# Optimization experiments

Hardware: AMD Instinct MI355X
Metric: run time of the kernel (lower is better)

Reference implementation:

```python
import jax, jax.numpy as jnp
import numpy as np

B, D, NH, HD, L, P, FF = 2, 256, 8, 32, 4, 4, 1024
SPATIAL = np.array([[100, 100], [50, 50], [25, 25], [13, 13]], dtype=np.int64)
S_TOTAL = int(SPATIAL.prod(1).sum())  # 13294
EPS = 1e-5


def setup_inputs() -> dict:
    key = jax.random.key(0)
    ks = jax.random.split(key, 20)
    std = 0.02
    f32 = jnp.float32
    return {
        "query": jax.random.normal(ks[0], (B, S_TOTAL, D), f32),
        "query_pos": jax.random.normal(ks[1], (B, S_TOTAL, D), f32),
        "valid_ratios": jnp.ones((B, L, 2), f32),
        "spatial_shapes": SPATIAL,
        "level_start_index": np.concatenate([[0], SPATIAL.prod(1).cumsum()[:-1]]).astype(np.int64),
        "W_off": jax.random.normal(ks[2], (D, NH * L * P * 2), f32) * std,
        "b_off": jax.random.normal(ks[3], (NH * L * P * 2,), f32) * std,
        "W_attn": jax.random.normal(ks[4], (D, NH * L * P), f32) * std,
        "b_attn": jax.random.normal(ks[5], (NH * L * P,), f32) * std,
        "W_val": jax.random.normal(ks[6], (D, D), f32) * std,
        "b_val": jnp.zeros((D,), f32),
        "W_out": jax.random.normal(ks[7], (D, D), f32) * std,
        "b_out": jnp.zeros((D,), f32),
        "ln1_g": jnp.ones((D,), f32),
        "ln1_b": jnp.zeros((D,), f32),
        "W1": jax.random.normal(ks[8], (D, FF), f32) * std,
        "b1": jnp.zeros((FF,), f32),
        "W2": jax.random.normal(ks[9], (FF, D), f32) * std,
        "b2": jnp.zeros((D,), f32),
        "ln2_g": jnp.ones((D,), f32),
        "ln2_b": jnp.zeros((D,), f32),
    }


def _layer_norm(x, g, b):
    m = x.mean(-1, keepdims=True)
    v = ((x - m) ** 2).mean(-1, keepdims=True)
    return (x - m) * jax.lax.rsqrt(v + EPS) * g + b


def _bilinear_sample(v, loc, H, W):
    # v: [B, NH, H*W, HD]; loc: [B, NH, S, P, 2] normalized to [0,1]
    # Matches F.grid_sample(bilinear, padding_mode='zeros', align_corners=False)
    x = loc[..., 0] * W - 0.5
    y = loc[..., 1] * H - 0.5
    x0 = jnp.floor(x)
    y0 = jnp.floor(y)
    lx, ly = x - x0, y - y0
    x0i = x0.astype(jnp.int32)
    y0i = y0.astype(jnp.int32)
    x1i, y1i = x0i + 1, y0i + 1

    def corner(yi, xi, w):
        valid = (xi >= 0) & (xi < W) & (yi >= 0) & (yi < H)
        idx = jnp.clip(yi, 0, H - 1) * W + jnp.clip(xi, 0, W - 1)  # [B,NH,S,P]
        b_, h_, s_, p_ = idx.shape
        g = jnp.take_along_axis(v, idx.reshape(b_, h_, s_ * p_)[..., None], axis=2)
        g = g.reshape(b_, h_, s_, p_, -1)
        return g * (w * valid)[..., None]

    return (corner(y0i, x0i, (1 - lx) * (1 - ly)) + corner(y0i, x1i, lx * (1 - ly))
            + corner(y1i, x0i, (1 - lx) * ly) + corner(y1i, x1i, lx * ly))


def _forward(query, query_pos, valid_ratios, spatial_shapes,
             W_off, b_off, W_attn, b_attn, W_val, b_val, W_out, b_out,
             ln1_g, ln1_b, W1, b1, W2, b2, ln2_g, ln2_b):
    ss = np.asarray(spatial_shapes)
    Bq, S, _ = query.shape

    # ----- reference points (per-pixel centers, normalized by valid ratios) -----
    refs = []
    for lvl in range(ss.shape[0]):
        H, W = int(ss[lvl, 0]), int(ss[lvl, 1])
        ry, rx = jnp.meshgrid(jnp.linspace(0.5, H - 0.5, H), jnp.linspace(0.5, W - 0.5, W), indexing='ij')
        vy = valid_ratios[:, lvl, 1][:, None, None]
        vx = valid_ratios[:, lvl, 0][:, None, None]
        ry = ry[None] / (vy * H)
        rx = rx[None] / (vx * W)
        refs.append(jnp.stack((rx, ry), -1).reshape(Bq, H * W, 2))
    ref = jnp.concatenate(refs, 1)  # [B, S, 2] (identical across levels)

    # ----- multi-scale deformable attention -----
    q = query + query_pos
    v = (query @ W_val + b_val).reshape(Bq, S, NH, HD).transpose(0, 2, 1, 3)  # [B,NH,S,HD]
    off = (q @ W_off + b_off).reshape(Bq, S, NH, L, P, 2)
    aw = jax.nn.softmax((q @ W_attn + b_attn).reshape(Bq, S, NH, L * P), -1)
    aw = aw.reshape(Bq, S, NH, L, P)
    normalizer = jnp.asarray(ss[:, ::-1].copy(), jnp.float32)  # (W, H) per level
    loc = ref[:, :, None, None, None, :] + off / normalizer[None, None, None, :, None, :]  # [B,S,NH,L,P,2]

    starts = np.concatenate([[0], ss.prod(1).cumsum()[:-1]])
    out = jnp.zeros((Bq, NH, S, HD), query.dtype)
    for lvl in range(ss.shape[0]):
        H, W = int(ss[lvl, 0]), int(ss[lvl, 1])
        s0 = int(starts[lvl])
        v_l = v[:, :, s0:s0 + H * W]                       # [B,NH,HW,HD]
        loc_l = loc[:, :, :, lvl].transpose(0, 2, 1, 3, 4)  # [B,NH,S,P,2]
        samp = _bilinear_sample(v_l, loc_l, H, W)           # [B,NH,S,P,HD]
        w_l = aw[:, :, :, lvl].transpose(0, 2, 1, 3)        # [B,NH,S,P]
        out = out + (samp * w_l[..., None]).sum(3)
    attn_out = out.transpose(0, 2, 1, 3).reshape(Bq, S, D) @ W_out + b_out

    # ----- residual + LN + FFN + residual + LN -----
    x = _layer_norm(query + attn_out, ln1_g, ln1_b)
    f = jax.nn.relu(x @ W1 + b1) @ W2 + b2
    return _layer_norm(x + f, ln2_g, ln2_b)


def reference(query, query_pos, valid_ratios, spatial_shapes, level_start_index,
              W_off, b_off, W_attn, b_attn, W_val, b_val, W_out, b_out,
              ln1_g, ln1_b, W1, b1, W2, b2, ln2_g, ln2_b):
    return _forward(query, query_pos, valid_ratios, spatial_shapes,
                    W_off, b_off, W_attn, b_attn, W_val, b_val, W_out, b_out,
                    ln1_g, ln1_b, W1, b1, W2, b2, ln2_g, ln2_b)
```

## Files before the change

kernel.cpp:

```cpp
#include <hip/hip_runtime.h>
#include <math.h>

#define R_ROWS 26588
#define S_TOT  13294
#define NHEAD  8
#define NLVL   4
#define EPSF   1e-5f

typedef __attribute__((ext_vector_type(8))) short short8;
typedef __attribute__((ext_vector_type(4))) float f32x4;
typedef __attribute__((ext_vector_type(2))) float f32x2;
typedef unsigned short ushort_t;

__device__ __forceinline__ unsigned short f2bf(float f) {
    unsigned int u = __builtin_bit_cast(unsigned int, f);
    unsigned int r = (u + 0x7FFFu + ((u >> 16) & 1u)) >> 16;
    return (unsigned short)r;
}

__global__ __launch_bounds__(256) void transpose_all_kernel(
    const float* __restrict__ W_val, const float* __restrict__ W_off,
    const float* __restrict__ W_attn, const float* __restrict__ W_out,
    const float* __restrict__ W1, const float* __restrict__ W2,
    ushort_t* __restrict__ wt_val, ushort_t* __restrict__ wt_off,
    ushort_t* __restrict__ wt_attn, ushort_t* __restrict__ wt_out,
    ushort_t* __restrict__ wt_w1, ushort_t* __restrict__ wt_w2)
{
    int bid = blockIdx.x;
    const float* src; ushort_t* dst; int K, N, t;
    if (bid < 64)       { src = W_val;  dst = wt_val;  K = 256;  N = 256;  t = bid; }
    else if (bid < 128) { src = W_off;  dst = wt_off;  K = 256;  N = 256;  t = bid - 64; }
    else if (bid < 160) { src = W_attn; dst = wt_attn; K = 256;  N = 128;  t = bid - 128; }
    else if (bid < 224) { src = W_out;  dst = wt_out;  K = 256;  N = 256;  t = bid - 160; }
    else if (bid < 480) { src = W1;     dst = wt_w1;   K = 256;  N = 1024; t = bid - 224; }
    else                { src = W2;     dst = wt_w2;   K = 1024; N = 256;  t = bid - 480; }
    int nt = N / 32;
    int bn = (t % nt) * 32, bk = (t / nt) * 32;

    __shared__ ushort_t tt[32][33];
    int x = threadIdx.x & 31;
    int y = threadIdx.x >> 5;
#pragma unroll
    for (int i = 0; i < 4; ++i) {
        int k = y + i * 8;
        tt[x][k] = f2bf(src[(long)(bk + k) * N + bn + x]);
    }
    __syncthreads();
#pragma unroll
    for (int i = 0; i < 4; ++i) {
        int n = y + i * 8;
        dst[(long)(bn + n) * K + bk + x] = tt[n][x];
    }
}

__global__ __launch_bounds__(256) void addcvt_kernel(
    const float* __restrict__ q, const float* __restrict__ p,
    ushort_t* __restrict__ qry_bf, ushort_t* __restrict__ qsum_bf, int n4)
{
    int i = blockIdx.x * 256 + threadIdx.x;
    if (i >= n4) return;
    float4 a = ((const float4*)q)[i];
    float4 b = ((const float4*)p)[i];
    uint2 qa, qs;
    qa.x = (unsigned)f2bf(a.x) | ((unsigned)f2bf(a.y) << 16);
    qa.y = (unsigned)f2bf(a.z) | ((unsigned)f2bf(a.w) << 16);
    qs.x = (unsigned)f2bf(a.x + b.x) | ((unsigned)f2bf(a.y + b.y) << 16);
    qs.y = (unsigned)f2bf(a.z + b.z) | ((unsigned)f2bf(a.w + b.w) << 16);
    ((uint2*)qry_bf)[i] = qa;
    ((uint2*)qsum_bf)[i] = qs;
}

__device__ __forceinline__ void stage32_async(
    const ushort_t* __restrict__ src_row0, int ld, int k0,
    ushort_t* lds, int wave, int lane)
{
#pragma unroll
    for (int inst = 0; inst < 2; ++inst) {
        int base_row = wave * 32 + inst * 16;
        int r = base_row + (lane >> 2);
        int quadS = lane & 3;
        int quadG = quadS ^ ((r >> 1) & 3);
        const ushort_t* gp = src_row0 + (long)r * ld + k0 + quadG * 8;
        __builtin_amdgcn_global_load_lds(
            (const __attribute__((address_space(1))) unsigned int*)gp,
            (__attribute__((address_space(3))) unsigned int*)&lds[base_row * 32],
            16, 0, 0);
    }
}

__device__ __forceinline__ void gemm_body(
    ushort_t* As, ushort_t* Bs,
    const ushort_t* __restrict__ A, const ushort_t* __restrict__ Wt,
    const float* __restrict__ bias, void* __restrict__ Cv,
    int M, int N, int K, int bm, int bn, bool out_bf16, bool relu)
{
    const int tid  = threadIdx.x;
    const int wave = tid >> 6;
    const int lane = tid & 63;
    const int l15  = lane & 15;
    const int quad = lane >> 4;
    const int wm   = (wave >> 1) * 64;
    const int wn   = (wave & 1) * 64;

    const ushort_t* Arow = A + (long)bm * K;
    const ushort_t* Brow = Wt + (long)bn * K;

    f32x4 acc[4][4];
#pragma unroll
    for (int i = 0; i < 4; ++i)
#pragma unroll
        for (int j = 0; j < 4; ++j) acc[i][j] = (f32x4)0.0f;

    int aoff[4], boff[4];
#pragma unroll
    for (int mi = 0; mi < 4; ++mi) {
        int r = wm + mi * 16 + l15;
        aoff[mi] = r * 32 + (quad ^ ((r >> 1) & 3)) * 8;
    }
#pragma unroll
    for (int ni = 0; ni < 4; ++ni) {
        int r = wn + ni * 16 + l15;
        boff[ni] = r * 32 + (quad ^ ((r >> 1) & 3)) * 8;
    }

    for (int k0 = 0; k0 < K; k0 += 32) {
        stage32_async(Arow, K, k0, As, wave, lane);
        stage32_async(Brow, K, k0, Bs, wave, lane);
        __syncthreads();

        short8 af[4], bf[4];
#pragma unroll
        for (int mi = 0; mi < 4; ++mi) af[mi] = *(const short8*)&As[aoff[mi]];
#pragma unroll
        for (int ni = 0; ni < 4; ++ni) bf[ni] = *(const short8*)&Bs[boff[ni]];
#pragma unroll
        for (int mi = 0; mi < 4; ++mi)
#pragma unroll
            for (int ni = 0; ni < 4; ++ni)
                acc[mi][ni] = __builtin_amdgcn_mfma_f32_16x16x32_bf16(
                    af[mi], bf[ni], acc[mi][ni], 0, 0, 0);
        __syncthreads();
    }

#pragma unroll
    for (int mi = 0; mi < 4; ++mi) {
#pragma unroll
        for (int r = 0; r < 4; ++r) {
            int row = bm + wm + mi * 16 + quad * 4 + r;
            if (row >= M) continue;
#pragma unroll
            for (int ni = 0; ni < 4; ++ni) {
                int col = bn + wn + ni * 16 + l15;
                float vv = acc[mi][ni][r] + bias[col];
                if (relu) vv = fmaxf(vv, 0.f);
                if (out_bf16)
                    ((ushort_t*)Cv)[(long)row * N + col] = f2bf(vv);
                else
                    ((float*)Cv)[(long)row * N + col] = vv;
            }
        }
    }
}

template<bool OUT_BF16, bool RELU>
__global__ __launch_bounds__(256) void gemm_mfma_kernel(
    const ushort_t* __restrict__ A, const ushort_t* __restrict__ Wt,
    const float* __restrict__ bias, void* __restrict__ Cv,
    int M, int N, int K)
{
    __shared__ ushort_t As[128 * 32];
    __shared__ ushort_t Bs[128 * 32];
    gemm_body(As, Bs, A, Wt, bias, Cv, M, N, K,
              blockIdx.x * 128, blockIdx.y * 128, OUT_BF16, RELU);
}

__global__ __launch_bounds__(256) void proj_kernel(
    const ushort_t* __restrict__ qry_bf, const ushort_t* __restrict__ q_bf,
    const ushort_t* __restrict__ wt_val, const ushort_t* __restrict__ wt_off,
    const ushort_t* __restrict__ wt_attn,
    const float* __restrict__ b_val, const float* __restrict__ b_off,
    const float* __restrict__ b_attn,
    ushort_t* __restrict__ v_bf, float* __restrict__ cb, float* __restrict__ logits)
{
    __shared__ ushort_t As[128 * 32];
    __shared__ ushort_t Bs[128 * 32];
    int y = blockIdx.y;
    const ushort_t* A; const ushort_t* Wt; const float* bias;
    void* C; bool outbf; int N, bn;
    if (y < 2)      { A = qry_bf; Wt = wt_val;  bias = b_val;  C = v_bf;   outbf = true;  N = 256; bn = y * 128; }
    else if (y < 4) { A = q_bf;   Wt = wt_off;  bias = b_off;  C = cb;     outbf = false; N = 256; bn = (y - 2) * 128; }
    else            { A = q_bf;   Wt = wt_attn; bias = b_attn; C = logits; outbf = false; N = 128; bn = 0; }
    gemm_body(As, Bs, A, Wt, bias, C, R_ROWS, N, 256, blockIdx.x * 128, bn, outbf, false);
}

__global__ __launch_bounds__(256) void deform_sample_kernel(
    const ushort_t* __restrict__ v, const float* __restrict__ off,
    const float* __restrict__ logits, const float* __restrict__ vr,
    ushort_t* __restrict__ out)
{
    const int Hs_[4] = {100, 50, 25, 13};
    const int S0_[4] = {0, 10000, 12500, 13125};

    int grp = blockIdx.x * 64 + (threadIdx.x >> 2);
    int j   = threadIdx.x & 3;
    if (grp >= R_ROWS * NHEAD) return;
    int h = grp & 7;
    int r = grp >> 3;
    int b = (r >= S_TOT) ? 1 : 0;
    int s = r - b * S_TOT;

    int lq = (s < 10000) ? 0 : (s < 12500) ? 1 : (s < 13125) ? 2 : 3;
    int t  = s - S0_[lq];
    int Wq = Hs_[lq];
    int iy = t / Wq;
    int jx = t - iy * Wq;
    float vx = vr[(b * NLVL + lq) * 2 + 0];
    float vy = vr[(b * NLVL + lq) * 2 + 1];
    float rx = (jx + 0.5f) / (vx * (float)Wq);
    float ry = (iy + 0.5f) / (vy * (float)Wq);

    const float* offp = off + (long)r * 256 + h * 32;
    float4 oa = ((const float4*)offp)[2 * j];
    float4 ob = ((const float4*)offp)[2 * j + 1];
    float4 lg = ((const float4*)(logits + (long)grp * 16))[j];

    float mx = fmaxf(fmaxf(lg.x, lg.y), fmaxf(lg.z, lg.w));
    mx = fmaxf(mx, __shfl_xor(mx, 1));
    mx = fmaxf(mx, __shfl_xor(mx, 2));
    float e0 = __expf(lg.x - mx), e1 = __expf(lg.y - mx);
    float e2 = __expf(lg.z - mx), e3 = __expf(lg.w - mx);
    float sum = e0 + e1 + e2 + e3;
    sum += __shfl_xor(sum, 1);
    sum += __shfl_xor(sum, 2);
    float inv = 1.f / sum;

    const int   H  = Hs_[j];
    const float fH = (float)H;
    const int   s0 = S0_[j];
    float oxs[4] = {oa.x, oa.z, ob.x, ob.z};
    float oys[4] = {oa.y, oa.w, ob.y, ob.w};
    float wts[4] = {e0 * inv, e1 * inv, e2 * inv, e3 * inv};
    float pw0[4], pw1[4], pw2[4], pw3[4];
    int   pi0[4], pi1[4], pi2[4], pi3[4];
#pragma unroll
    for (int i = 0; i < 4; ++i) {
        float x = rx * fH + oxs[i] - 0.5f;
        float y = ry * fH + oys[i] - 0.5f;
        float xf = floorf(x), yf = floorf(y);
        float lx = x - xf, ly = y - yf;
        int x0 = (int)xf, y0 = (int)yf;
        bool xv0 = (x0 >= 0) & (x0 < H);
        bool xv1 = (x0 >= -1) & (x0 < H - 1);
        bool yv0 = (y0 >= 0) & (y0 < H);
        bool yv1 = (y0 >= -1) & (y0 < H - 1);
        float w = wts[i];
        pw0[i] = (xv0 & yv0) ? (1.f - lx) * (1.f - ly) * w : 0.f;
        pw1[i] = (xv1 & yv0) ? lx * (1.f - ly) * w : 0.f;
        pw2[i] = (xv0 & yv1) ? (1.f - lx) * ly * w : 0.f;
        pw3[i] = (xv1 & yv1) ? lx * ly * w : 0.f;
        int xc0 = min(max(x0, 0), H - 1), xc1 = min(max(x0 + 1, 0), H - 1);
        int yc0 = min(max(y0, 0), H - 1), yc1 = min(max(y0 + 1, 0), H - 1);
        pi0[i] = s0 + yc0 * H + xc0;
        pi1[i] = s0 + yc0 * H + xc1;
        pi2[i] = s0 + yc1 * H + xc0;
        pi3[i] = s0 + yc1 * H + xc1;
    }

    const ushort_t* vb = v + ((long)b * S_TOT) * 256 + h * 32 + j * 8;
    f32x2 acc2[4];
#pragma unroll
    for (int c = 0; c < 4; ++c) acc2[c] = (f32x2)0.0f;

#define ACC_CORNER(IDX, WGT) do {                                            \
        uint4 g = *(const uint4*)&vb[(long)(IDX) * 256];                     \
        unsigned uu0 = g.x, uu1 = g.y, uu2 = g.z, uu3 = g.w;                 \
        f32x2 gv;                                                            \
        gv.x = __builtin_bit_cast(float, uu0 << 16);                         \
        gv.y = __builtin_bit_cast(float, uu0 & 0xFFFF0000u);                 \
        acc2[0] += gv * (WGT);                                               \
        gv.x = __builtin_bit_cast(float, uu1 << 16);                         \
        gv.y = __builtin_bit_cast(float, uu1 & 0xFFFF0000u);                 \
        acc2[1] += gv * (WGT);                                               \
        gv.x = __builtin_bit_cast(float, uu2 << 16);                         \
        gv.y = __builtin_bit_cast(float, uu2 & 0xFFFF0000u);                 \
        acc2[2] += gv * (WGT);                                               \
        gv.x = __builtin_bit_cast(float, uu3 << 16);                         \
        gv.y = __builtin_bit_cast(float, uu3 & 0xFFFF0000u);                 \
        acc2[3] += gv * (WGT);                                               \
    } while (0)

#pragma unroll
    for (int i = 0; i < 4; ++i) {
#pragma unroll
        for (int j2 = 0; j2 < 4; ++j2) {
            float w00 = __shfl(pw0[i], j2, 4);
            float w01 = __shfl(pw1[i], j2, 4);
            float w10 = __shfl(pw2[i], j2, 4);
            float w11 = __shfl(pw3[i], j2, 4);
            int   i00 = __shfl(pi0[i], j2, 4);
            int   i01 = __shfl(pi1[i], j2, 4);
            int   i10 = __shfl(pi2[i], j2, 4);
            int   i11 = __shfl(pi3[i], j2, 4);
            ACC_CORNER(i00, w00);
            ACC_CORNER(i01, w01);
            ACC_CORNER(i10, w10);
            ACC_CORNER(i11, w11);
        }
    }
#undef ACC_CORNER

    uint4 o;
    o.x = (unsigned)f2bf(acc2[0].x) | ((unsigned)f2bf(acc2[0].y) << 16);
    o.y = (unsigned)f2bf(acc2[1].x) | ((unsigned)f2bf(acc2[1].y) << 16);
    o.z = (unsigned)f2bf(acc2[2].x) | ((unsigned)f2bf(acc2[2].y) << 16);
    o.w = (unsigned)f2bf(acc2[3].x) | ((unsigned)f2bf(acc2[3].y) << 16);
    *(uint4*)&out[(long)r * 256 + h * 32 + j * 8] = o;
}

template<bool DUAL>
__global__ __launch_bounds__(256) void add_ln_kernel(
    const float* __restrict__ a, const float* __restrict__ b,
    const float* __restrict__ g, const float* __restrict__ beta,
    float* __restrict__ outf, ushort_t* __restrict__ outb)
{
    int row = blockIdx.x;
    int tid = threadIdx.x;
    float x = a[(long)row * 256 + tid] + b[(long)row * 256 + tid];
    float s1 = x, s2 = x * x;
#pragma unroll
    for (int o = 32; o > 0; o >>= 1) {
        s1 += __shfl_down(s1, o, 64);
        s2 += __shfl_down(s2, o, 64);
    }
    __shared__ float sh1[4], sh2[4];
    int w = tid >> 6;
    if ((tid & 63) == 0) { sh1[w] = s1; sh2[w] = s2; }
    __syncthreads();
    float t1 = sh1[0] + sh1[1] + sh1[2] + sh1[3];
    float t2 = sh2[0] + sh2[1] + sh2[2] + sh2[3];
    float mean = t1 * (1.f / 256.f);
    float var  = t2 * (1.f / 256.f) - mean * mean;
    float inv  = rsqrtf(var + EPSF);
    float y = (x - mean) * inv * g[tid] + beta[tid];
    outf[(long)row * 256 + tid] = y;
    if (DUAL) outb[(long)row * 256 + tid] = f2bf(y);
}

extern "C" void kernel_launch(void* const* d_in, const int* in_sizes, int n_in,
                              void* d_out, int out_size, void* d_ws, size_t ws_size,
                              hipStream_t stream)
{
    const float* query  = (const float*)d_in[0];
    const float* qpos   = (const float*)d_in[1];
    const float* vr     = (const float*)d_in[2];
    const float* W_off  = (const float*)d_in[5];
    const float* b_off  = (const float*)d_in[6];
    const float* W_attn = (const float*)d_in[7];
    const float* b_attn = (const float*)d_in[8];
    const float* W_val  = (const float*)d_in[9];
    const float* b_val  = (const float*)d_in[10];
    const float* W_out  = (const float*)d_in[11];
    const float* b_out  = (const float*)d_in[12];
    const float* ln1g   = (const float*)d_in[13];
    const float* ln1b   = (const float*)d_in[14];
    const float* W1     = (const float*)d_in[15];
    const float* b1     = (const float*)d_in[16];
    const float* W2     = (const float*)d_in[17];
    const float* b2     = (const float*)d_in[18];
    const float* ln2g   = (const float*)d_in[19];
    const float* ln2b   = (const float*)d_in[20];
    float* out = (float*)d_out;

    float* ws = (float*)d_ws;
    const long R128 = (long)R_ROWS * 128;
    ushort_t* q_bf    = (ushort_t*)(ws);
    ushort_t* qry_bf  = (ushort_t*)(ws + R128);
    ushort_t* v_bf    = (ushort_t*)(ws + 2 * R128);
    float*    logits  = ws + 3 * R128;
    ushort_t* h_bf    = (ushort_t*)(ws);
    float*    cb      = ws + 4 * R128;
    ushort_t* samp_bf = (ushort_t*)(ws + 6 * R128);
    float*    xb      = ws + 7 * R128;
    ushort_t* wt      = (ushort_t*)(ws + 9 * R128);
    ushort_t* wt_val  = wt;
    ushort_t* wt_off  = wt + 65536;
    ushort_t* wt_attn = wt + 131072;
    ushort_t* wt_out  = wt + 163840;
    ushort_t* wt_w1   = wt + 229376;
    ushort_t* wt_w2   = wt + 491520;

    dim3 blk(256);
    const int MB = (R_ROWS + 127) / 128;

    transpose_all_kernel<<<736, blk, 0, stream>>>(
        W_val, W_off, W_attn, W_out, W1, W2,
        wt_val, wt_off, wt_attn, wt_out, wt_w1, wt_w2);
    addcvt_kernel<<<(R_ROWS * 64 + 255) / 256, blk, 0, stream>>>(
        query, qpos, qry_bf, q_bf, R_ROWS * 64);
    proj_kernel<<<dim3(MB, 5), blk, 0, stream>>>(
        qry_bf, q_bf, wt_val, wt_off, wt_attn, b_val, b_off, b_attn,
        v_bf, cb, logits);
    deform_sample_kernel<<<(R_ROWS * NHEAD + 63) / 64, blk, 0, stream>>>(
        v_bf, cb, logits, vr, samp_bf);
    gemm_mfma_kernel<false, false><<<dim3(MB, 2), blk, 0, stream>>>(
        samp_bf, wt_out, b_out, cb, R_ROWS, 256, 256);
    add_ln_kernel<true><<<R_ROWS, blk, 0, stream>>>(query, cb, ln1g, ln1b, xb, samp_bf);
    gemm_mfma_kernel<true, true><<<dim3(MB, 8), blk, 0, stream>>>(
        samp_bf, wt_w1, b1, h_bf, R_ROWS, 1024, 256);
    gemm_mfma_kernel<false, false><<<dim3(MB, 2), blk, 0, stream>>>(
        h_bf, wt_w2, b2, cb, R_ROWS, 256, 1024);
    add_ln_kernel<false><<<R_ROWS, blk, 0, stream>>>(xb, cb, ln2g, ln2b, out, nullptr);
}
```

Before: 333.4 us.

## Triple-buffer GEMM LDS staging and remap deform-sample blocks across XCDs

The shared GEMM body now prefetches the next K-slice into one of three LDS buffers while computing on the current one. It waits with an explicit vmcnt and a single raw s_barrier instead of two __syncthreads per iteration. The deformable sampling kernel remaps blockIdx so that the 8 round-robin XCD slots each get a contiguous chunk of rows, aiming for better L2 locality. This triples LDS use per block, which can reduce occupancy, and the single-barrier three-buffer scheme depends on the vmcnt counts being right.

```diff
diff --git a/kernel.cpp b/kernel.cpp
--- a/kernel.cpp
+++ b/kernel.cpp
@@ -70,20 +70,34 @@
     ((uint2*)qsum_bf)[i] = qs;
 }
 
-__device__ __forceinline__ void stage32_async(
-    const ushort_t* __restrict__ src_row0, int ld, int k0,
-    ushort_t* lds, int wave, int lane)
-{
+#define TBUF 4096
+
+__device__ __forceinline__ void stage_ab(
+    const ushort_t* __restrict__ Arow, const ushort_t* __restrict__ Brow,
+    int K, int k0, ushort_t* As, ushort_t* Bs, int wave, int lane)
+{
+    int quadS = lane & 3;
+    int rr = lane >> 2;
 #pragma unroll
     for (int inst = 0; inst < 2; ++inst) {
         int base_row = wave * 32 + inst * 16;
-        int r = base_row + (lane >> 2);
-        int quadS = lane & 3;
+        int r = base_row + rr;
         int quadG = quadS ^ ((r >> 1) & 3);
-        const ushort_t* gp = src_row0 + (long)r * ld + k0 + quadG * 8;
+        const ushort_t* gp = Arow + (long)r * K + k0 + quadG * 8;
         __builtin_amdgcn_global_load_lds(
             (const __attribute__((address_space(1))) unsigned int*)gp,
-            (__attribute__((address_space(3))) unsigned int*)&lds[base_row * 32],
+            (__attribute__((address_space(3))) unsigned int*)&As[base_row * 32],
+            16, 0, 0);
+    }
+#pragma unroll
+    for (int inst = 0; inst < 2; ++inst) {
+        int base_row = wave * 32 + inst * 16;
+        int r = base_row + rr;
+        int quadG = quadS ^ ((r >> 1) & 3);
+        const ushort_t* gp = Brow + (long)r * K + k0 + quadG * 8;
+        __builtin_amdgcn_global_load_lds(
+            (const __attribute__((address_space(1))) unsigned int*)gp,
+            (__attribute__((address_space(3))) unsigned int*)&Bs[base_row * 32],
             16, 0, 0);
     }
 }
@@ -123,23 +137,34 @@
         boff[ni] = r * 32 + (quad ^ ((r >> 1) & 3)) * 8;
     }
 
-    for (int k0 = 0; k0 < K; k0 += 32) {
-        stage32_async(Arow, K, k0, As, wave, lane);
-        stage32_async(Brow, K, k0, Bs, wave, lane);
-        __syncthreads();
-
+    const int NT = K >> 5;
+    stage_ab(Arow, Brow, K, 0, As, Bs, wave, lane);
+    int cur = 0;
+    for (int t = 0; t < NT; ++t) {
+        int nxt = cur + 1; if (nxt == 3) nxt = 0;
+        if (t + 1 < NT) {
+            stage_ab(Arow, Brow, K, (t + 1) << 5,
+                     As + nxt * TBUF, Bs + nxt * TBUF, wave, lane);
+            asm volatile("s_waitcnt vmcnt(4)" ::: "memory");
+        } else {
+            asm volatile("s_waitcnt vmcnt(0)" ::: "memory");
+        }
+        asm volatile("s_barrier" ::: "memory");
+
+        const ushort_t* Ab = As + cur * TBUF;
+        const ushort_t* Bb = Bs + cur * TBUF;
         short8 af[4], bf[4];
 #pragma unroll
-        for (int mi = 0; mi < 4; ++mi) af[mi] = *(const short8*)&As[aoff[mi]];
-#pragma unroll
-        for (int ni = 0; ni < 4; ++ni) bf[ni] = *(const short8*)&Bs[boff[ni]];
+        for (int mi = 0; mi < 4; ++mi) af[mi] = *(const short8*)&Ab[aoff[mi]];
+#pragma unroll
+        for (int ni = 0; ni < 4; ++ni) bf[ni] = *(const short8*)&Bb[boff[ni]];
 #pragma unroll
         for (int mi = 0; mi < 4; ++mi)
 #pragma unroll
             for (int ni = 0; ni < 4; ++ni)
                 acc[mi][ni] = __builtin_amdgcn_mfma_f32_16x16x32_bf16(
                     af[mi], bf[ni], acc[mi][ni], 0, 0, 0);
-        __syncthreads();
+        cur = nxt;
     }
 
 #pragma unroll
@@ -168,8 +193,8 @@
     const float* __restrict__ bias, void* __restrict__ Cv,
     int M, int N, int K)
 {
-    __shared__ ushort_t As[128 * 32];
-    __shared__ ushort_t Bs[128 * 32];
+    __shared__ ushort_t As[3 * TBUF];
+    __shared__ ushort_t Bs[3 * TBUF];
     gemm_body(As, Bs, A, Wt, bias, Cv, M, N, K,
               blockIdx.x * 128, blockIdx.y * 128, OUT_BF16, RELU);
 }
@@ -182,8 +207,8 @@
     const float* __restrict__ b_attn,
     ushort_t* __restrict__ v_bf, float* __restrict__ cb, float* __restrict__ logits)
 {
-    __shared__ ushort_t As[128 * 32];
-    __shared__ ushort_t Bs[128 * 32];
+    __shared__ ushort_t As[3 * TBUF];
+    __shared__ ushort_t Bs[3 * TBUF];
     int y = blockIdx.y;
     const ushort_t* A; const ushort_t* Wt; const float* bias;
     void* C; bool outbf; int N, bn;
@@ -193,6 +218,9 @@
     gemm_body(As, Bs, A, Wt, bias, C, R_ROWS, N, 256, blockIdx.x * 128, bn, outbf, false);
 }
 
+#define DEF_BLOCKS 3328
+#define DEF_CHUNK  416
+
 __global__ __launch_bounds__(256) void deform_sample_kernel(
     const ushort_t* __restrict__ v, const float* __restrict__ off,
     const float* __restrict__ logits, const float* __restrict__ vr,
@@ -201,7 +229,8 @@
     const int Hs_[4] = {100, 50, 25, 13};
     const int S0_[4] = {0, 10000, 12500, 13125};
 
-    int grp = blockIdx.x * 64 + (threadIdx.x >> 2);
+    int wb  = (blockIdx.x & 7) * DEF_CHUNK + (blockIdx.x >> 3);
+    int grp = wb * 64 + (threadIdx.x >> 2);
     int j   = threadIdx.x & 3;
     if (grp >= R_ROWS * NHEAD) return;
     int h = grp & 7;
@@ -400,7 +429,7 @@
     proj_kernel<<<dim3(MB, 5), blk, 0, stream>>>(
         qry_bf, q_bf, wt_val, wt_off, wt_attn, b_val, b_off, b_attn,
         v_bf, cb, logits);
-    deform_sample_kernel<<<(R_ROWS * NHEAD + 63) / 64, blk, 0, stream>>>(
+    deform_sample_kernel<<<DEF_BLOCKS, blk, 0, stream>>>(
         v_bf, cb, logits, vr, samp_bf);
     gemm_mfma_kernel<false, false><<<dim3(MB, 2), blk, 0, stream>>>(
         samp_bf, wt_out, b_out, cb, R_ROWS, 256, 256);
```

Measured after the change: 326.9 us. 1.02x faster.
